# Performance work log

Measured on AMD Instinct MI355X. Metric: run time of the kernel, lower is better.

The kernel has to match this reference:

```python
import jax, jax.numpy as jnp
import numpy as np

B, T, D = 8, 2048, 1024
H, N = 8, 32  # n_heads, n_state


def _xavier(key, shape, fan_in, fan_out):
    lim = float(np.sqrt(6.0 / (fan_in + fan_out)))
    return jax.random.uniform(key, shape, jnp.float32, -lim, lim)


def setup_inputs() -> dict:
    key = jax.random.key(0)
    ks = jax.random.split(key, 8)
    x = jax.random.normal(ks[0], (B, T, D), jnp.float32)
    W_in = _xavier(ks[1], (D, D), D, D)                    # in_proj.weight [d_inner, dim]
    # per-head xavier on [n_state, d_inner] slices -> limit sqrt(6/(N+D))
    W_k = _xavier(ks[2], (H * N, D), N, D)
    W_v = _xavier(ks[3], (H * N, D), N, D)
    W_q = _xavier(ks[4], (H * N, D), N, D)
    W_beta = _xavier(ks[5], (H * N, D), N, D)
    b_beta = jnp.full((H, N), 2.0, jnp.float32)            # init_beta_bias
    W_out = _xavier(ks[6], (D, H * N), H * N, D)           # out_proj.weight [dim, H*n]
    return {"x": x, "W_in": W_in, "W_k": W_k, "W_v": W_v, "W_q": W_q,
            "W_beta": W_beta, "b_beta": b_beta, "W_out": W_out}


def reference(x, W_in, W_k, W_v, W_q, W_beta, b_beta, W_out):
    b, t, d = x.shape
    h, n = b_beta.shape
    # in_proj + SiLU (use_conv=False)
    xp = jax.nn.silu(jnp.einsum('btd,ed->bte', x, W_in))   # [B,T,D_inner]
    def proj(W):  # -> [T,B,H,N]
        return jnp.einsum('btd,md->btm', xp, W).reshape(b, t, h, n).transpose(1, 0, 2, 3)
    k_all = proj(W_k)
    v_all = proj(W_v)
    q_all = proj(W_q)
    beta_all = jax.nn.sigmoid(proj(W_beta) + b_beta)       # [T,B,H,N]

    S0 = jnp.zeros((b, h, n, n), x.dtype)

    def step(S, inp):
        k, v, q, beta = inp                                 # each [B,H,N]
        kn = k / (jnp.linalg.norm(k, axis=-1, keepdims=True) + 1e-6)
        retrieved = jnp.einsum('bhij,bhj->bhi', S, kn)
        delta = v - retrieved
        S = jnp.tanh(beta[..., None] * S + delta[..., None] * kn[..., None, :])
        Sq = jnp.einsum('bhij,bhj->bhi', S, q)
        out = Sq * jax.nn.silu(Sq)                          # [B,H,N]
        return S, out

    S_final, outs = jax.lax.scan(step, S0, (k_all, v_all, q_all, beta_all))
    cell_out = outs.transpose(1, 0, 2, 3).reshape(b, t, h * n)  # [B,T,H*N]
    y = jnp.einsum('btm,dm->btd', cell_out, W_out)          # out_proj, no bias
    return y, S_final
```

## Files before the change

### kernel.cpp

```cpp
#include <hip/hip_runtime.h>
#include <hip/hip_bf16.h>

#define TT 2048
#define BB 8
#define HH 8
#define NNS 32
#define MM (BB * TT)
#define CH 16

typedef __attribute__((ext_vector_type(8))) short short8;
typedef __attribute__((ext_vector_type(4))) float f32x4;

__device__ __forceinline__ float bf2f(ushort u) {
    return __uint_as_float(((unsigned)u) << 16);
}
__device__ __forceinline__ ushort f2bf(float f) {
    unsigned x = __float_as_uint(f);
    unsigned r = (x + 0x7fffu + ((x >> 16) & 1u)) >> 16;
    return (ushort)r;
}
__device__ __forceinline__ float sigmoidf_fast(float x) {
    float e = __builtin_amdgcn_exp2f(x * -1.4426950408889634f);
    return __builtin_amdgcn_rcpf(1.0f + e);
}
__device__ __forceinline__ float tanhf_fast(float x) {
    float e = __builtin_amdgcn_exp2f(x * 2.8853900817779268f);
    return fmaf(-2.0f, __builtin_amdgcn_rcpf(e + 1.0f), 1.0f);
}

__device__ __forceinline__ void gl16(const void* g, void* l) {
    auto gp = (const __attribute__((address_space(1))) unsigned int*)g;
    auto lp = (__attribute__((address_space(3))) unsigned int*)l;
    __builtin_amdgcn_global_load_lds(gp, lp, 16, 0, 0);
}

template<int CTRL>
__device__ __forceinline__ float dpp_add(float x) {
    int y = __builtin_amdgcn_update_dpp(0, __float_as_int(x), CTRL, 0xF, 0xF, true);
    return x + __int_as_float(y);
}
__device__ __forceinline__ float red16(float x) {
    x = dpp_add<0xB1>(x);
    x = dpp_add<0x4E>(x);
    x = dpp_add<0x124>(x);
    x = dpp_add<0x128>(x);
    return x;
}

__device__ __forceinline__ void split8(const float4& x0, const float4& x1,
                                       ushort* __restrict__ h, ushort* __restrict__ l) {
    float xs[8] = {x0.x, x0.y, x0.z, x0.w, x1.x, x1.y, x1.z, x1.w};
#pragma unroll
    for (int i = 0; i < 8; ++i) {
        ushort hh = f2bf(xs[i]);
        h[i] = hh;
        l[i] = f2bf(xs[i] - bf2f(hh));
    }
}

__global__ __launch_bounds__(256) void conv_x_kernel(
    const float* __restrict__ src, ushort* __restrict__ hi, ushort* __restrict__ lo)
{
    size_t e = ((size_t)blockIdx.x * 256 + threadIdx.x) * 8;
    float4 x0 = *reinterpret_cast<const float4*>(src + e);
    float4 x1 = *reinterpret_cast<const float4*>(src + e + 4);
    ushort h[8], l[8];
    split8(x0, x1, h, l);
    *reinterpret_cast<uint4*>(hi + e) = *reinterpret_cast<const uint4*>(h);
    *reinterpret_cast<uint4*>(lo + e) = *reinterpret_cast<const uint4*>(l);
}

__global__ __launch_bounds__(256) void conv_w_kernel(
    const float* __restrict__ Wi, const float* __restrict__ Wk,
    const float* __restrict__ Wv, const float* __restrict__ Wq,
    const float* __restrict__ Wb, const float* __restrict__ Wo,
    ushort* __restrict__ W1h, ushort* __restrict__ W1l,
    ushort* __restrict__ W2h, ushort* __restrict__ W2l,
    ushort* __restrict__ W3h)
{
    size_t e = ((size_t)blockIdx.x * 256 + threadIdx.x) * 8;
    const float* s;
    ushort* dh; ushort* dl; size_t doff; bool dolo = true;
    if (e < 1048576) {
        s = Wi + e; dh = W1h; dl = W1l; doff = e;
    } else if (e < 2097152) {
        size_t u = e - 1048576;
        int wi = (int)(u >> 18);
        const float* sp = (wi == 0) ? Wk : (wi == 1) ? Wv : (wi == 2) ? Wq : Wb;
        s = sp + (u & 262143); dh = W2h; dl = W2l; doff = u;
    } else {
        size_t u = e - 2097152;
        s = Wo + u; dh = W3h; dl = nullptr; doff = u; dolo = false;
    }
    float4 x0 = *reinterpret_cast<const float4*>(s);
    float4 x1 = *reinterpret_cast<const float4*>(s + 4);
    ushort h[8], l[8];
    split8(x0, x1, h, l);
    *reinterpret_cast<uint4*>(dh + doff) = *reinterpret_cast<const uint4*>(h);
    if (dolo)
        *reinterpret_cast<uint4*>(dl + doff) = *reinterpret_cast<const uint4*>(l);
}

template<int ACT>
__global__ __launch_bounds__(256, 3) void gemm_planes(
    const ushort* __restrict__ Ah_g, const ushort* __restrict__ Al_g,
    const ushort* __restrict__ Wh_g, const ushort* __restrict__ Wl_g,
    const float* __restrict__ bbeta,
    ushort* __restrict__ Ch, ushort* __restrict__ Cl,
    float* __restrict__ Cf, int M, int N, int K)
{
    __shared__ __align__(16) ushort sAh[128][32], sAl[128][32];
    __shared__ __align__(16) ushort sWh[128][32], sWl[128][32];
    const int t = threadIdx.x;
    const int wave = t >> 6, lane = t & 63;
    const int lr = lane & 15, lq = lane >> 4;
    const int wm = wave >> 1, wn = wave & 1;

    const int bid = blockIdx.y * 8 + blockIdx.x;
    const int swz = (bid & 7) * 128 + (bid >> 3);
    const int n0 = (swz & 7) * 128;
    const int m0 = (swz >> 3) * 128;

    const int rs0 = wave * 32 + (lane >> 2);
    const int rs1 = rs0 + 16;
    const int ce  = (lane & 3) * 8;
    const ushort* gA0h = Ah_g + (size_t)(m0 + rs0) * K + ce;
    const ushort* gA1h = Ah_g + (size_t)(m0 + rs1) * K + ce;
    const ushort* gA0l = Al_g + (size_t)(m0 + rs0) * K + ce;
    const ushort* gA1l = Al_g + (size_t)(m0 + rs1) * K + ce;
    const ushort* gW0h = Wh_g + (size_t)(n0 + rs0) * K + ce;
    const ushort* gW1h = Wh_g + (size_t)(n0 + rs1) * K + ce;
    const ushort* gW0l = Wl_g + (size_t)(n0 + rs0) * K + ce;
    const ushort* gW1l = Wl_g + (size_t)(n0 + rs1) * K + ce;
    const int lb = wave * 2048 + lane * 16;
    char* LAh = (char*)&sAh[0][0];
    char* LAl = (char*)&sAl[0][0];
    char* LWh = (char*)&sWh[0][0];
    char* LWl = (char*)&sWl[0][0];

    f32x4 acc[4][4];
#pragma unroll
    for (int mi = 0; mi < 4; ++mi)
#pragma unroll
        for (int ni = 0; ni < 4; ++ni) acc[mi][ni] = (f32x4){0.f, 0.f, 0.f, 0.f};

    const int NK = K >> 5;
    for (int ks = 0; ks < NK; ++ks) {
        const int k0 = ks << 5;
        __syncthreads();
        gl16(gA0h + k0, LAh + lb);  gl16(gA1h + k0, LAh + lb + 1024);
        gl16(gA0l + k0, LAl + lb);  gl16(gA1l + k0, LAl + lb + 1024);
        gl16(gW0h + k0, LWh + lb);  gl16(gW1h + k0, LWh + lb + 1024);
        gl16(gW0l + k0, LWl + lb);  gl16(gW1l + k0, LWl + lb + 1024);
        __syncthreads();
        short8 ah[4], al[4], wh[4], wl[4];
#pragma unroll
        for (int mi = 0; mi < 4; ++mi) {
            ah[mi] = *reinterpret_cast<const short8*>(&sAh[wm * 64 + mi * 16 + lr][lq * 8]);
            al[mi] = *reinterpret_cast<const short8*>(&sAl[wm * 64 + mi * 16 + lr][lq * 8]);
        }
#pragma unroll
        for (int ni = 0; ni < 4; ++ni) {
            wh[ni] = *reinterpret_cast<const short8*>(&sWh[wn * 64 + ni * 16 + lr][lq * 8]);
            wl[ni] = *reinterpret_cast<const short8*>(&sWl[wn * 64 + ni * 16 + lr][lq * 8]);
        }
#pragma unroll
        for (int mi = 0; mi < 4; ++mi) {
#pragma unroll
            for (int ni = 0; ni < 4; ++ni) {
                acc[mi][ni] = __builtin_amdgcn_mfma_f32_16x16x32_bf16(ah[mi], wh[ni], acc[mi][ni], 0, 0, 0);
                acc[mi][ni] = __builtin_amdgcn_mfma_f32_16x16x32_bf16(ah[mi], wl[ni], acc[mi][ni], 0, 0, 0);
                acc[mi][ni] = __builtin_amdgcn_mfma_f32_16x16x32_bf16(al[mi], wh[ni], acc[mi][ni], 0, 0, 0);
            }
        }
    }

#pragma unroll
    for (int mi = 0; mi < 4; ++mi) {
#pragma unroll
        for (int ni = 0; ni < 4; ++ni) {
#pragma unroll
            for (int r2 = 0; r2 < 4; ++r2) {
                int mg = m0 + wm * 64 + mi * 16 + lq * 4 + r2;
                int ng = n0 + wn * 64 + ni * 16 + lr;
                float v = acc[mi][ni][r2];
                if (ACT == 1) {
                    v = v * sigmoidf_fast(v);
                    ushort h = f2bf(v);
                    ushort lo_ = f2bf(v - bf2f(h));
                    Ch[(size_t)mg * N + ng] = h;
                    Cl[(size_t)mg * N + ng] = lo_;
                } else {
                    if (ACT == 2 && ng >= 768) v = sigmoidf_fast(v + bbeta[ng - 768]);
                    Cf[(size_t)mg * N + ng] = v;
                }
            }
        }
    }
}

__global__ __launch_bounds__(256, 4) void gemm_cell(
    const ushort* __restrict__ A, const ushort* __restrict__ Wh_g,
    float* __restrict__ C, int M, int N, int K)
{
    __shared__ __align__(16) ushort sA[128][32];
    __shared__ __align__(16) ushort sW[128][32];
    const int t = threadIdx.x;
    const int wave = t >> 6, lane = t & 63;
    const int lr = lane & 15, lq = lane >> 4;
    const int wm = wave >> 1, wn = wave & 1;

    const int bid = blockIdx.y * 8 + blockIdx.x;
    const int swz = (bid & 7) * 128 + (bid >> 3);
    const int n0 = (swz & 7) * 128;
    const int m0 = (swz >> 3) * 128;

    const int rs0 = wave * 32 + (lane >> 2);
    const int rs1 = rs0 + 16;
    const int ce  = (lane & 3) * 8;
    const ushort* gA0 = A    + (size_t)(m0 + rs0) * K + ce;
    const ushort* gA1 = A    + (size_t)(m0 + rs1) * K + ce;
    const ushort* gW0 = Wh_g + (size_t)(n0 + rs0) * K + ce;
    const ushort* gW1 = Wh_g + (size_t)(n0 + rs1) * K + ce;
    const int lb = wave * 2048 + lane * 16;
    char* LA = (char*)&sA[0][0];
    char* LW = (char*)&sW[0][0];

    f32x4 acc[4][4];
#pragma unroll
    for (int mi = 0; mi < 4; ++mi)
#pragma unroll
        for (int ni = 0; ni < 4; ++ni) acc[mi][ni] = (f32x4){0.f, 0.f, 0.f, 0.f};

    const int NK = K >> 5;
    for (int ks = 0; ks < NK; ++ks) {
        const int k0 = ks << 5;
        __syncthreads();
        gl16(gA0 + k0, LA + lb);  gl16(gA1 + k0, LA + lb + 1024);
        gl16(gW0 + k0, LW + lb);  gl16(gW1 + k0, LW + lb + 1024);
        __syncthreads();
        short8 af[4], wf[4];
#pragma unroll
        for (int mi = 0; mi < 4; ++mi)
            af[mi] = *reinterpret_cast<const short8*>(&sA[wm * 64 + mi * 16 + lr][lq * 8]);
#pragma unroll
        for (int ni = 0; ni < 4; ++ni)
            wf[ni] = *reinterpret_cast<const short8*>(&sW[wn * 64 + ni * 16 + lr][lq * 8]);
#pragma unroll
        for (int mi = 0; mi < 4; ++mi)
#pragma unroll
            for (int ni = 0; ni < 4; ++ni)
                acc[mi][ni] = __builtin_amdgcn_mfma_f32_16x16x32_bf16(af[mi], wf[ni], acc[mi][ni], 0, 0, 0);
    }

#pragma unroll
    for (int mi = 0; mi < 4; ++mi) {
#pragma unroll
        for (int ni = 0; ni < 4; ++ni) {
#pragma unroll
            for (int r2 = 0; r2 < 4; ++r2) {
                int mg = m0 + wm * 64 + mi * 16 + lq * 4 + r2;
                int ng = n0 + wn * 64 + ni * 16 + lr;
                C[(size_t)mg * N + ng] = acc[mi][ni][r2];
            }
        }
    }
}

__global__ __launch_bounds__(256) void kn_kernel(
    const float* __restrict__ P, float* __restrict__ KN)
{
    int idx = blockIdx.x * 256 + threadIdx.x;
    int col = idx & 255;
    int bt  = idx >> 8;
    float k = P[(size_t)bt * 1024 + col];
    float ks = k * k;
    ks += __shfl_xor(ks, 1, 32);  ks += __shfl_xor(ks, 2, 32);
    ks += __shfl_xor(ks, 4, 32);  ks += __shfl_xor(ks, 8, 32);
    ks += __shfl_xor(ks, 16, 32);
    KN[idx] = k * __builtin_amdgcn_rcpf(sqrtf(ks) + 1e-6f);
}

__device__ __forceinline__ void lds_load8(
    float (&K_)[CH][32], float (&Q_)[CH][32], float (&VB)[CH][8],
    int base, int l, int iw,
    float (&k0)[8], float (&k1)[8], float (&q0)[8], float (&q1)[8],
    float (&vv)[8], float (&bb)[8])
{
#pragma unroll
    for (int u = 0; u < 8; ++u) {
        k0[u] = K_[base + u][l];  k1[u] = K_[base + u][l + 16];
        q0[u] = Q_[base + u][l];  q1[u] = Q_[base + u][l + 16];
        vv[u] = VB[base + u][iw]; bb[u] = VB[base + u][iw + 4];
    }
}

__device__ __forceinline__ void steps8(
    float (&k0)[8], float (&k1)[8], float (&q0)[8], float (&q1)[8],
    float (&vv)[8], float (&bb)[8],
    float& S0, float& S1, float (&sqp)[8])
{
#pragma unroll
    for (int u = 0; u < 8; ++u) {
        float p = red16(fmaf(S0, k0[u], S1 * k1[u]));
        float delta = vv[u] - p;
        S0 = tanhf_fast(fmaf(bb[u], S0, delta * k0[u]));
        S1 = tanhf_fast(fmaf(bb[u], S1, delta * k1[u]));
        sqp[u] = fmaf(S0, q0[u], S1 * q1[u]);
    }
}

__device__ __forceinline__ void flush8(
    float (&sqp)[8], ushort* __restrict__ cell, size_t crow, int l)
{
    float r0 = red16(sqp[0]), r1 = red16(sqp[1]);
    float r2 = red16(sqp[2]), r3 = red16(sqp[3]);
    float r4 = red16(sqp[4]), r5 = red16(sqp[5]);
    float r6 = red16(sqp[6]), r7 = red16(sqp[7]);
    if (l < 8) {
        float s01 = (l & 1) ? r1 : r0;
        float s23 = (l & 1) ? r3 : r2;
        float s45 = (l & 1) ? r5 : r4;
        float s67 = (l & 1) ? r7 : r6;
        float a03 = (l & 2) ? s23 : s01;
        float a47 = (l & 2) ? s67 : s45;
        float sel = (l & 4) ? a47 : a03;
        float o = sel * sel * sigmoidf_fast(sel);
        cell[crow + (size_t)l * 256] = f2bf(o);
    }
}

template<int DO_STAGE>
__device__ __forceinline__ void scan_chunk16(
    float (&K_)[CH][32], float (&Q_)[CH][32], float (&VB)[CH][8],
    float (&NK)[CH][32], float (&NQ)[CH][32], float (&NVB)[CH][8],
    const float*& gkn, const float*& gq, const float*& gv, const float*& gb,
    float (&k0A)[8], float (&k1A)[8], float (&q0A)[8], float (&q1A)[8],
    float (&vvA)[8], float (&bbA)[8],
    float (&k0B)[8], float (&k1B)[8], float (&q0B)[8], float (&q1B)[8],
    float (&vvB)[8], float (&bbB)[8],
    float& S0, float& S1, float (&sqp)[8],
    ushort* __restrict__ cell, size_t crow, int l, int iw, int j)
{
    float4 Lk0, Lk1, Lq0, Lq1;
    float Lv = 0.f, Lb = 0.f;
    if (DO_STAGE) {
        Lk0 = *reinterpret_cast<const float4*>(gkn);
        Lk1 = *reinterpret_cast<const float4*>(gkn + 8 * 256);
        Lq0 = *reinterpret_cast<const float4*>(gq);
        Lq1 = *reinterpret_cast<const float4*>(gq + 8 * 1024);
        Lv  = *gv;
        Lb  = *gb;
        gkn += CH * 256; gq += CH * 1024; gv += CH * 1024; gb += CH * 1024;
    }
    lds_load8(K_, Q_, VB, 8, l, iw, k0B, k1B, q0B, q1B, vvB, bbB);
    steps8(k0A, k1A, q0A, q1A, vvA, bbA, S0, S1, sqp);
    flush8(sqp, cell, crow, l);
    if (DO_STAGE) {
        *reinterpret_cast<float4*>(&NK[j >> 3][(j & 7) * 4]) = Lk0;
        *reinterpret_cast<float4*>(&NK[8 + (j >> 3)][(j & 7) * 4]) = Lk1;
        *reinterpret_cast<float4*>(&NQ[j >> 3][(j & 7) * 4]) = Lq0;
        *reinterpret_cast<float4*>(&NQ[8 + (j >> 3)][(j & 7) * 4]) = Lq1;
        NVB[j >> 2][j & 3] = Lv;
        NVB[j >> 2][4 + (j & 3)] = Lb;
        lds_load8(NK, NQ, NVB, 0, l, iw, k0A, k1A, q0A, q1A, vvA, bbA);
    }
    steps8(k0B, k1B, q0B, q1B, vvB, bbB, S0, S1, sqp);
    flush8(sqp, cell, crow + (size_t)8 * 256, l);
}

__global__ __launch_bounds__(64, 1) void scan_kernel(
    const float* __restrict__ P,
    const float* __restrict__ KN,
    ushort* __restrict__ cell,
    float* __restrict__ Sout)
{
    const int b    = blockIdx.x & 7;
    const int r    = blockIdx.x >> 3;
    const int h    = r & 7;
    const int quad = r >> 3;
    const int j    = threadIdx.x;
    const int l    = j & 15;
    const int iw   = j >> 4;
    const int i    = quad * 4 + iw;

    __shared__ __align__(16) float sK0[CH][32], sK1[CH][32];
    __shared__ __align__(16) float sQ0[CH][32], sQ1[CH][32];
    __shared__ __align__(16) float sVB0[CH][8], sVB1[CH][8];

    const size_t bt0 = (size_t)b * TT;
    const float* gkn = KN + (bt0 + (j >> 3)) * 256 + h * 32 + (j & 7) * 4;
    const float* gq  = P  + (bt0 + (j >> 3)) * 1024 + 512 + h * 32 + (j & 7) * 4;
    const float* gv  = P  + (bt0 + (j >> 2)) * 1024 + 256 + h * 32 + quad * 4 + (j & 3);
    const float* gb  = P  + (bt0 + (j >> 2)) * 1024 + 768 + h * 32 + quad * 4 + (j & 3);

    float k0A[8], k1A[8], q0A[8], q1A[8], vvA[8], bbA[8];
    float k0B[8], k1B[8], q0B[8], q1B[8], vvB[8], bbB[8];
    float sqp[8];
    float S0 = 0.f, S1 = 0.f;
    const size_t cb = (size_t)b * TT * 256 + h * 32 + i;

    {
        float4 K0v = *reinterpret_cast<const float4*>(gkn);
        float4 K1v = *reinterpret_cast<const float4*>(gkn + 8 * 256);
        float4 Q0v = *reinterpret_cast<const float4*>(gq);
        float4 Q1v = *reinterpret_cast<const float4*>(gq + 8 * 1024);
        float v0 = *gv, b0 = *gb;
        gkn += CH * 256; gq += CH * 1024; gv += CH * 1024; gb += CH * 1024;
        *reinterpret_cast<float4*>(&sK0[j >> 3][(j & 7) * 4]) = K0v;
        *reinterpret_cast<float4*>(&sK0[8 + (j >> 3)][(j & 7) * 4]) = K1v;
        *reinterpret_cast<float4*>(&sQ0[j >> 3][(j & 7) * 4]) = Q0v;
        *reinterpret_cast<float4*>(&sQ0[8 + (j >> 3)][(j & 7) * 4]) = Q1v;
        sVB0[j >> 2][j & 3] = v0;
        sVB0[j >> 2][4 + (j & 3)] = b0;
    }
    lds_load8(sK0, sQ0, sVB0, 0, l, iw, k0A, k1A, q0A, q1A, vvA, bbA);

    size_t crow = cb;
    for (int c = 0; c < 63; ++c) {
        scan_chunk16<1>(sK0, sQ0, sVB0, sK1, sQ1, sVB1,
                        gkn, gq, gv, gb,
                        k0A, k1A, q0A, q1A, vvA, bbA,
                        k0B, k1B, q0B, q1B, vvB, bbB,
                        S0, S1, sqp, cell, crow, l, iw, j);
        crow += (size_t)CH * 256;
        scan_chunk16<1>(sK1, sQ1, sVB1, sK0, sQ0, sVB0,
                        gkn, gq, gv, gb,
                        k0A, k1A, q0A, q1A, vvA, bbA,
                        k0B, k1B, q0B, q1B, vvB, bbB,
                        S0, S1, sqp, cell, crow, l, iw, j);
        crow += (size_t)CH * 256;
    }
    scan_chunk16<1>(sK0, sQ0, sVB0, sK1, sQ1, sVB1,
                    gkn, gq, gv, gb,
                    k0A, k1A, q0A, q1A, vvA, bbA,
                    k0B, k1B, q0B, q1B, vvB, bbB,
                    S0, S1, sqp, cell, crow, l, iw, j);
    crow += (size_t)CH * 256;
    scan_chunk16<0>(sK1, sQ1, sVB1, sK0, sQ0, sVB0,
                    gkn, gq, gv, gb,
                    k0A, k1A, q0A, q1A, vvA, bbA,
                    k0B, k1B, q0B, q1B, vvB, bbB,
                    S0, S1, sqp, cell, crow, l, iw, j);

    float* so = Sout + (((size_t)(b * HH + h)) * NNS + i) * NNS;
    so[l] = S0;
    so[l + 16] = S1;
}

extern "C" void kernel_launch(void* const* d_in, const int* in_sizes, int n_in,
                              void* d_out, int out_size, void* d_ws, size_t ws_size,
                              hipStream_t stream) {
    const float* x     = (const float*)d_in[0];
    const float* W_in  = (const float*)d_in[1];
    const float* W_k   = (const float*)d_in[2];
    const float* W_v   = (const float*)d_in[3];
    const float* W_q   = (const float*)d_in[4];
    const float* W_b   = (const float*)d_in[5];
    const float* b_b   = (const float*)d_in[6];
    const float* W_out = (const float*)d_in[7];
    float* out = (float*)d_out;

    const int M = MM;
    float* f = (float*)d_ws;
    float*  P    = f;
    ushort* Xh   = (ushort*)f;
    ushort* Xl   = Xh + (size_t)M * 1024;
    ushort* xpH  = (ushort*)(f + (size_t)M * 1024);
    ushort* xpL  = xpH + (size_t)M * 1024;
    float*  KN   = f + (size_t)2 * M * 1024;
    ushort* cell = (ushort*)(KN + (size_t)M * 256);
    ushort* wb   = cell + (size_t)M * 256;
    ushort* W1h = wb;
    ushort* W1l = W1h + 1048576;
    ushort* W2h = W1l + 1048576;
    ushort* W2l = W2h + 1048576;
    ushort* W3h = W2l + 1048576;

    dim3 blk(256);
    dim3 g1(1024 / 128, M / 128);

    conv_x_kernel<<<dim3((M * 1024) / (8 * 256)), blk, 0, stream>>>(x, Xh, Xl);
    conv_w_kernel<<<dim3(2359296 / (8 * 256)), blk, 0, stream>>>(
        W_in, W_k, W_v, W_q, W_b, W_out, W1h, W1l, W2h, W2l, W3h);
    gemm_planes<1><<<g1, blk, 0, stream>>>(Xh, Xl, W1h, W1l, b_b,
                                           xpH, xpL, nullptr, M, 1024, 1024);
    gemm_planes<2><<<g1, blk, 0, stream>>>(xpH, xpL, W2h, W2l, b_b,
                                           nullptr, nullptr, P, M, 1024, 1024);
    kn_kernel<<<dim3((M * 256) / 256), blk, 0, stream>>>(P, KN);
    scan_kernel<<<dim3(512), dim3(64), 0, stream>>>(P, KN, cell, out + (size_t)M * 1024);
    gemm_cell<<<g1, blk, 0, stream>>>(cell, W3h, out, M, 1024, 256);
}
```

Baseline: 569.1 us.

## Process two state rows per scan thread to give each wavefront two independent chains

```diff
diff --git a/kernel.cpp b/kernel.cpp
--- a/kernel.cpp
+++ b/kernel.cpp
@@ -281,32 +281,39 @@
     KN[idx] = k * __builtin_amdgcn_rcpf(sqrtf(ks) + 1e-6f);
 }
 
-__device__ __forceinline__ void lds_load8(
-    float (&K_)[CH][32], float (&Q_)[CH][32], float (&VB)[CH][8],
+__device__ __forceinline__ void lds_load8d(
+    float (&K_)[CH][32], float (&Q_)[CH][32], float (&VB)[CH][16],
     int base, int l, int iw,
     float (&k0)[8], float (&k1)[8], float (&q0)[8], float (&q1)[8],
-    float (&vv)[8], float (&bb)[8])
+    float (&vx)[8], float (&bx)[8], float (&vy)[8], float (&by)[8])
 {
 #pragma unroll
     for (int u = 0; u < 8; ++u) {
         k0[u] = K_[base + u][l];  k1[u] = K_[base + u][l + 16];
         q0[u] = Q_[base + u][l];  q1[u] = Q_[base + u][l + 16];
-        vv[u] = VB[base + u][iw]; bb[u] = VB[base + u][iw + 4];
-    }
-}
-
-__device__ __forceinline__ void steps8(
+        vx[u] = VB[base + u][iw];      vy[u] = VB[base + u][4 + iw];
+        bx[u] = VB[base + u][8 + iw];  by[u] = VB[base + u][12 + iw];
+    }
+}
+
+__device__ __forceinline__ void steps8d(
     float (&k0)[8], float (&k1)[8], float (&q0)[8], float (&q1)[8],
-    float (&vv)[8], float (&bb)[8],
-    float& S0, float& S1, float (&sqp)[8])
+    float (&vx)[8], float (&bx)[8], float (&vy)[8], float (&by)[8],
+    float& SX0, float& SX1, float& SY0, float& SY1,
+    float (&sqx)[8], float (&sqy)[8])
 {
 #pragma unroll
     for (int u = 0; u < 8; ++u) {
-        float p = red16(fmaf(S0, k0[u], S1 * k1[u]));
-        float delta = vv[u] - p;
-        S0 = tanhf_fast(fmaf(bb[u], S0, delta * k0[u]));
-        S1 = tanhf_fast(fmaf(bb[u], S1, delta * k1[u]));
-        sqp[u] = fmaf(S0, q0[u], S1 * q1[u]);
+        float px = red16(fmaf(SX0, k0[u], SX1 * k1[u]));
+        float py = red16(fmaf(SY0, k0[u], SY1 * k1[u]));
+        float dx = vx[u] - px;
+        float dy = vy[u] - py;
+        SX0 = tanhf_fast(fmaf(bx[u], SX0, dx * k0[u]));
+        SX1 = tanhf_fast(fmaf(bx[u], SX1, dx * k1[u]));
+        SY0 = tanhf_fast(fmaf(by[u], SY0, dy * k0[u]));
+        SY1 = tanhf_fast(fmaf(by[u], SY1, dy * k1[u]));
+        sqx[u] = fmaf(SX0, q0[u], SX1 * q1[u]);
+        sqy[u] = fmaf(SY0, q0[u], SY1 * q1[u]);
     }
 }
 
@@ -331,42 +338,48 @@
 }
 
 template<int DO_STAGE>
-__device__ __forceinline__ void scan_chunk16(
-    float (&K_)[CH][32], float (&Q_)[CH][32], float (&VB)[CH][8],
-    float (&NK)[CH][32], float (&NQ)[CH][32], float (&NVB)[CH][8],
-    const float*& gkn, const float*& gq, const float*& gv, const float*& gb,
+__device__ __forceinline__ void scan_chunk16d(
+    float (&K_)[CH][32], float (&Q_)[CH][32], float (&VB)[CH][16],
+    float (&NK)[CH][32], float (&NQ)[CH][32], float (&NVB)[CH][16],
+    const float*& gkn, const float*& gq,
+    const float*& gvx, const float*& gvy, const float*& gbx, const float*& gby,
     float (&k0A)[8], float (&k1A)[8], float (&q0A)[8], float (&q1A)[8],
-    float (&vvA)[8], float (&bbA)[8],
+    float (&vxA)[8], float (&bxA)[8], float (&vyA)[8], float (&byA)[8],
     float (&k0B)[8], float (&k1B)[8], float (&q0B)[8], float (&q1B)[8],
-    float (&vvB)[8], float (&bbB)[8],
-    float& S0, float& S1, float (&sqp)[8],
-    ushort* __restrict__ cell, size_t crow, int l, int iw, int j)
+    float (&vxB)[8], float (&bxB)[8], float (&vyB)[8], float (&byB)[8],
+    float& SX0, float& SX1, float& SY0, float& SY1,
+    float (&sqx)[8], float (&sqy)[8],
+    ushort* __restrict__ cell, size_t crowX, size_t crowY, int l, int iw, int j)
 {
     float4 Lk0, Lk1, Lq0, Lq1;
-    float Lv = 0.f, Lb = 0.f;
+    float Lvx = 0.f, Lvy = 0.f, Lbx = 0.f, Lby = 0.f;
     if (DO_STAGE) {
         Lk0 = *reinterpret_cast<const float4*>(gkn);
         Lk1 = *reinterpret_cast<const float4*>(gkn + 8 * 256);
         Lq0 = *reinterpret_cast<const float4*>(gq);
         Lq1 = *reinterpret_cast<const float4*>(gq + 8 * 1024);
-        Lv  = *gv;
-        Lb  = *gb;
-        gkn += CH * 256; gq += CH * 1024; gv += CH * 1024; gb += CH * 1024;
-    }
-    lds_load8(K_, Q_, VB, 8, l, iw, k0B, k1B, q0B, q1B, vvB, bbB);
-    steps8(k0A, k1A, q0A, q1A, vvA, bbA, S0, S1, sqp);
-    flush8(sqp, cell, crow, l);
+        Lvx = *gvx;  Lvy = *gvy;  Lbx = *gbx;  Lby = *gby;
+        gkn += CH * 256; gq += CH * 1024;
+        gvx += CH * 1024; gvy += CH * 1024; gbx += CH * 1024; gby += CH * 1024;
+    }
+    lds_load8d(K_, Q_, VB, 8, l, iw, k0B, k1B, q0B, q1B, vxB, bxB, vyB, byB);
+    steps8d(k0A, k1A, q0A, q1A, vxA, bxA, vyA, byA, SX0, SX1, SY0, SY1, sqx, sqy);
+    flush8(sqx, cell, crowX, l);
+    flush8(sqy, cell, crowY, l);
     if (DO_STAGE) {
         *reinterpret_cast<float4*>(&NK[j >> 3][(j & 7) * 4]) = Lk0;
         *reinterpret_cast<float4*>(&NK[8 + (j >> 3)][(j & 7) * 4]) = Lk1;
         *reinterpret_cast<float4*>(&NQ[j >> 3][(j & 7) * 4]) = Lq0;
         *reinterpret_cast<float4*>(&NQ[8 + (j >> 3)][(j & 7) * 4]) = Lq1;
-        NVB[j >> 2][j & 3] = Lv;
-        NVB[j >> 2][4 + (j & 3)] = Lb;
-        lds_load8(NK, NQ, NVB, 0, l, iw, k0A, k1A, q0A, q1A, vvA, bbA);
-    }
-    steps8(k0B, k1B, q0B, q1B, vvB, bbB, S0, S1, sqp);
-    flush8(sqp, cell, crow + (size_t)8 * 256, l);
+        NVB[j >> 2][j & 3]        = Lvx;
+        NVB[j >> 2][4 + (j & 3)]  = Lvy;
+        NVB[j >> 2][8 + (j & 3)]  = Lbx;
+        NVB[j >> 2][12 + (j & 3)] = Lby;
+        lds_load8d(NK, NQ, NVB, 0, l, iw, k0A, k1A, q0A, q1A, vxA, bxA, vyA, byA);
+    }
+    steps8d(k0B, k1B, q0B, q1B, vxB, bxB, vyB, byB, SX0, SX1, SY0, SY1, sqx, sqy);
+    flush8(sqx, cell, crowX + (size_t)8 * 256, l);
+    flush8(sqy, cell, crowY + (size_t)8 * 256, l);
 }
 
 __global__ __launch_bounds__(64, 1) void scan_kernel(
@@ -375,77 +388,91 @@
     ushort* __restrict__ cell,
     float* __restrict__ Sout)
 {
-    const int b    = blockIdx.x & 7;
-    const int r    = blockIdx.x >> 3;
-    const int h    = r & 7;
-    const int quad = r >> 3;
-    const int j    = threadIdx.x;
-    const int l    = j & 15;
-    const int iw   = j >> 4;
-    const int i    = quad * 4 + iw;
+    const int b  = blockIdx.x & 7;
+    const int r  = blockIdx.x >> 3;
+    const int h  = r & 7;
+    const int qp = r >> 3;
+    const int j  = threadIdx.x;
+    const int l  = j & 15;
+    const int iw = j >> 4;
+    const int iX = qp * 4 + iw;
+    const int iY = iX + 16;
 
     __shared__ __align__(16) float sK0[CH][32], sK1[CH][32];
     __shared__ __align__(16) float sQ0[CH][32], sQ1[CH][32];
-    __shared__ __align__(16) float sVB0[CH][8], sVB1[CH][8];
+    __shared__ __align__(16) float sVB0[CH][16], sVB1[CH][16];
 
     const size_t bt0 = (size_t)b * TT;
     const float* gkn = KN + (bt0 + (j >> 3)) * 256 + h * 32 + (j & 7) * 4;
     const float* gq  = P  + (bt0 + (j >> 3)) * 1024 + 512 + h * 32 + (j & 7) * 4;
-    const float* gv  = P  + (bt0 + (j >> 2)) * 1024 + 256 + h * 32 + quad * 4 + (j & 3);
-    const float* gb  = P  + (bt0 + (j >> 2)) * 1024 + 768 + h * 32 + quad * 4 + (j & 3);
-
-    float k0A[8], k1A[8], q0A[8], q1A[8], vvA[8], bbA[8];
-    float k0B[8], k1B[8], q0B[8], q1B[8], vvB[8], bbB[8];
-    float sqp[8];
-    float S0 = 0.f, S1 = 0.f;
-    const size_t cb = (size_t)b * TT * 256 + h * 32 + i;
+    const float* gvx = P  + (bt0 + (j >> 2)) * 1024 + 256 + h * 32 + qp * 4 + (j & 3);
+    const float* gvy = gvx + 16;
+    const float* gbx = P  + (bt0 + (j >> 2)) * 1024 + 768 + h * 32 + qp * 4 + (j & 3);
+    const float* gby = gbx + 16;
+
+    float k0A[8], k1A[8], q0A[8], q1A[8], vxA[8], bxA[8], vyA[8], byA[8];
+    float k0B[8], k1B[8], q0B[8], q1B[8], vxB[8], bxB[8], vyB[8], byB[8];
+    float sqx[8], sqy[8];
+    float SX0 = 0.f, SX1 = 0.f, SY0 = 0.f, SY1 = 0.f;
+    const size_t cbX = (size_t)b * TT * 256 + h * 32 + iX;
+    const size_t cbY = cbX + 16;
 
     {
         float4 K0v = *reinterpret_cast<const float4*>(gkn);
         float4 K1v = *reinterpret_cast<const float4*>(gkn + 8 * 256);
         float4 Q0v = *reinterpret_cast<const float4*>(gq);
         float4 Q1v = *reinterpret_cast<const float4*>(gq + 8 * 1024);
-        float v0 = *gv, b0 = *gb;
-        gkn += CH * 256; gq += CH * 1024; gv += CH * 1024; gb += CH * 1024;
+        float vx0 = *gvx, vy0 = *gvy, bx0 = *gbx, by0 = *gby;
+        gkn += CH * 256; gq += CH * 1024;
+        gvx += CH * 1024; gvy += CH * 1024; gbx += CH * 1024; gby += CH * 1024;
         *reinterpret_cast<float4*>(&sK0[j >> 3][(j & 7) * 4]) = K0v;
         *reinterpret_cast<float4*>(&sK0[8 + (j >> 3)][(j & 7) * 4]) = K1v;
         *reinterpret_cast<float4*>(&sQ0[j >> 3][(j & 7) * 4]) = Q0v;
         *reinterpret_cast<float4*>(&sQ0[8 + (j >> 3)][(j & 7) * 4]) = Q1v;
-        sVB0[j >> 2][j & 3] = v0;
-        sVB0[j >> 2][4 + (j & 3)] = b0;
-    }
-    lds_load8(sK0, sQ0, sVB0, 0, l, iw, k0A, k1A, q0A, q1A, vvA, bbA);
-
-    size_t crow = cb;
+        sVB0[j >> 2][j & 3]        = vx0;
+        sVB0[j >> 2][4 + (j & 3)]  = vy0;
+        sVB0[j >> 2][8 + (j & 3)]  = bx0;
+        sVB0[j >> 2][12 + (j & 3)] = by0;
+    }
+    lds_load8d(sK0, sQ0, sVB0, 0, l, iw, k0A, k1A, q0A, q1A, vxA, bxA, vyA, byA);
+
+    size_t crowX = cbX, crowY = cbY;
     for (int c = 0; c < 63; ++c) {
-        scan_chunk16<1>(sK0, sQ0, sVB0, sK1, sQ1, sVB1,
-                        gkn, gq, gv, gb,
-                        k0A, k1A, q0A, q1A, vvA, bbA,
-                        k0B, k1B, q0B, q1B, vvB, bbB,
-                        S0, S1, sqp, cell, crow, l, iw, j);
-        crow += (size_t)CH * 256;
-        scan_chunk16<1>(sK1, sQ1, sVB1, sK0, sQ0, sVB0,
-                        gkn, gq, gv, gb,
-                        k0A, k1A, q0A, q1A, vvA, bbA,
-                        k0B, k1B, q0B, q1B, vvB, bbB,
-                        S0, S1, sqp, cell, crow, l, iw, j);
-        crow += (size_t)CH * 256;
-    }
-    scan_chunk16<1>(sK0, sQ0, sVB0, sK1, sQ1, sVB1,
-                    gkn, gq, gv, gb,
-                    k0A, k1A, q0A, q1A, vvA, bbA,
-                    k0B, k1B, q0B, q1B, vvB, bbB,
-                    S0, S1, sqp, cell, crow, l, iw, j);
-    crow += (size_t)CH * 256;
-    scan_chunk16<0>(sK1, sQ1, sVB1, sK0, sQ0, sVB0,
-                    gkn, gq, gv, gb,
-                    k0A, k1A, q0A, q1A, vvA, bbA,
-                    k0B, k1B, q0B, q1B, vvB, bbB,
-                    S0, S1, sqp, cell, crow, l, iw, j);
-
-    float* so = Sout + (((size_t)(b * HH + h)) * NNS + i) * NNS;
-    so[l] = S0;
-    so[l + 16] = S1;
+        scan_chunk16d<1>(sK0, sQ0, sVB0, sK1, sQ1, sVB1,
+                         gkn, gq, gvx, gvy, gbx, gby,
+                         k0A, k1A, q0A, q1A, vxA, bxA, vyA, byA,
+                         k0B, k1B, q0B, q1B, vxB, bxB, vyB, byB,
+                         SX0, SX1, SY0, SY1, sqx, sqy,
+                         cell, crowX, crowY, l, iw, j);
+        crowX += (size_t)CH * 256;  crowY += (size_t)CH * 256;
+        scan_chunk16d<1>(sK1, sQ1, sVB1, sK0, sQ0, sVB0,
+                         gkn, gq, gvx, gvy, gbx, gby,
+                         k0A, k1A, q0A, q1A, vxA, bxA, vyA, byA,
+                         k0B, k1B, q0B, q1B, vxB, bxB, vyB, byB,
+                         SX0, SX1, SY0, SY1, sqx, sqy,
+                         cell, crowX, crowY, l, iw, j);
+        crowX += (size_t)CH * 256;  crowY += (size_t)CH * 256;
+    }
+    scan_chunk16d<1>(sK0, sQ0, sVB0, sK1, sQ1, sVB1,
+                     gkn, gq, gvx, gvy, gbx, gby,
+                     k0A, k1A, q0A, q1A, vxA, bxA, vyA, byA,
+                     k0B, k1B, q0B, q1B, vxB, bxB, vyB, byB,
+                     SX0, SX1, SY0, SY1, sqx, sqy,
+                     cell, crowX, crowY, l, iw, j);
+    crowX += (size_t)CH * 256;  crowY += (size_t)CH * 256;
+    scan_chunk16d<0>(sK1, sQ1, sVB1, sK0, sQ0, sVB0,
+                     gkn, gq, gvx, gvy, gbx, gby,
+                     k0A, k1A, q0A, q1A, vxA, bxA, vyA, byA,
+                     k0B, k1B, q0B, q1B, vxB, bxB, vyB, byB,
+                     SX0, SX1, SY0, SY1, sqx, sqy,
+                     cell, crowX, crowY, l, iw, j);
+
+    float* soX = Sout + (((size_t)(b * HH + h)) * NNS + iX) * NNS;
+    soX[l] = SX0;
+    soX[l + 16] = SX1;
+    float* soY = Sout + (((size_t)(b * HH + h)) * NNS + iY) * NNS;
+    soY[l] = SY0;
+    soY[l + 16] = SY1;
 }
 
 extern "C" void kernel_launch(void* const* d_in, const int* in_sizes, int n_in,
@@ -488,6 +515,6 @@
     gemm_planes<2><<<g1, blk, 0, stream>>>(xpH, xpL, W2h, W2l, b_b,
                                            nullptr, nullptr, P, M, 1024, 1024);
     kn_kernel<<<dim3((M * 256) / 256), blk, 0, stream>>>(P, KN);
-    scan_kernel<<<dim3(512), dim3(64), 0, stream>>>(P, KN, cell, out + (size_t)M * 1024);
+    scan_kernel<<<dim3(256), dim3(64), 0, stream>>>(P, KN, cell, out + (size_t)M * 1024);
     gemm_cell<<<g1, blk, 0, stream>>>(cell, W3h, out, M, 1024, 256);
 }
```

Result: slower. 689.3 us (+21.1%).
